# Optimization experiments

Measured on AMD Instinct MI355X. Metric: run time of the kernel, lower is better.

Reference implementation:

```python
import jax, jax.numpy as jnp
import numpy as np

B, T, LAGS, H, F = 4096, 256, 32, 128, 2


def setup_inputs() -> dict:
    key = jax.random.key(0)
    ks = jax.random.split(key, 6)
    s = lambda n: 1.0 / np.sqrt(n)
    return {
        "inputs": jax.random.normal(ks[0], (B, T, F), jnp.float32),
        "Wx": jax.random.normal(ks[1], (F, H), jnp.float32) * s(F),
        "Wh": jax.random.normal(ks[2], (H, H), jnp.float32) * s(H),
        "b": jnp.zeros((H,), jnp.float32),
        "Wd": jax.random.normal(ks[3], (H, 1), jnp.float32) * s(H),
        "bd": jnp.zeros((1,), jnp.float32),
        "alpha": jax.random.uniform(ks[4], (1, 1), jnp.float32),
        "lags": LAGS,
    }


def reference(inputs, Wx, Wh, b, Wd, bd, alpha, lags):
    # alpha constrained to [0, 1] (MinMax constraint / clamp in call)
    a = jnp.clip(alpha, 0.0, 1.0)  # [1,1]
    Bsz = inputs.shape[0]
    h0 = jnp.zeros((Bsz, Wh.shape[0]), inputs.dtype)

    def cell(h, x):
        # SimpleRNN cell: tanh(x Wx + h Wh + b)
        return jnp.tanh(x @ Wx + h @ Wh + b)

    # ---- warmup: run RNN over first `lags` steps of the full 2-feature input
    warm_xs = jnp.transpose(inputs[:, :lags], (1, 0, 2))  # [lags, B, F]

    def warm_step(h, x):
        return cell(h, x), None

    h, _ = jax.lax.scan(warm_step, h0, warm_xs)
    pred = h @ Wd + bd  # [B, 1] first prediction (appended un-smoothed)

    # step n consumes exogenous inputs[:, lags + n - 1, 0]
    exog = jnp.transpose(inputs[:, lags:-1, 0])  # [T-lags-1, B]

    def ar_step(carry, e):
        h, pred, es = carry
        x = jnp.concatenate([e[:, None], pred], axis=-1)  # [B, 2]
        h = cell(h, x)
        pred = h @ Wd + bd
        es = a * pred + (1.0 - a) * es  # exponential smoothing blend
        return (h, pred, es), es

    _, es_seq = jax.lax.scan(ar_step, (h, pred, pred), exog)  # [T-lags-1, B, 1]

    preds = jnp.concatenate([pred[None], es_seq], axis=0)  # [T-lags, B, 1]
    return jnp.transpose(preds, (1, 0, 2))  # [B, T-lags, 1]
```

## Files before the change

kernel.cpp:

```cpp
#include <hip/hip_runtime.h>

namespace {

constexpr int kB = 4096;
constexpr int kT = 256;
constexpr int kLags = 32;
constexpr int kH = 128;
constexpr int kSteps = 255;
constexpr int kOut = 224;
constexpr int kMT = 16;
constexpr int kThreads = 512;
constexpr int kHS = 136;
constexpr int kOS = 225;

constexpr float kZS = 2.8853900817779268f;

typedef __attribute__((ext_vector_type(8))) short short8;
typedef __attribute__((ext_vector_type(4))) float f32x4;

struct __align__(16) SMem {
    unsigned short hhi[2][kMT][kHS];
    unsigned short hlo[2][kMT][kHS];
    float x0T[kT][kMT];
    float x1wT[kLags][kMT];
    float obuf[kMT][kOS];
};

__device__ __forceinline__ unsigned short bf16_rne(float f) {
    unsigned u = __builtin_bit_cast(unsigned, f);
    u += 0x7FFFu + ((u >> 16) & 1u);
    return (unsigned short)(u >> 16);
}
__device__ __forceinline__ float bf16_f32(unsigned short h) {
    unsigned u = ((unsigned)h) << 16;
    return __builtin_bit_cast(float, u);
}
__device__ __forceinline__ float tanh_from_zs(float zs) {
    float e = __builtin_amdgcn_exp2f(zs);
    return fmaf(-2.0f, __builtin_amdgcn_rcpf(e + 1.0f), 1.0f);
}
__device__ __forceinline__ unsigned bf16_rne_hibits(float f) {
    unsigned u = __builtin_bit_cast(unsigned, f);
    return (u + (0x7FFFu + ((u >> 16) & 1u))) & 0xFFFF0000u;
}

__global__ __launch_bounds__(kThreads, 2)
void arx_rnn_es_kernel(const float* __restrict__ inputs,
                       const float* __restrict__ Wx,
                       const float* __restrict__ Wh,
                       const float* __restrict__ bias,
                       const float* __restrict__ Wd,
                       const float* __restrict__ bd,
                       const float* __restrict__ alpha,
                       float* __restrict__ out) {
    __shared__ SMem sm;
    const int tid  = threadIdx.x;
    const int b0   = blockIdx.x * kMT;
    const int lane = tid & 63;
    const int w    = tid >> 6;
    const int n    = lane & 15;
    const int q    = lane >> 4;

    for (int idx = tid; idx < kMT * kT; idx += kThreads) {
        const int mm = idx >> 8;
        const int t  = idx & 255;
        float2 v = ((const float2*)inputs)[(size_t)(b0 + mm) * kT + t];
        sm.x0T[t][mm] = v.x;
        if (t < kLags) sm.x1wT[t][mm] = v.y;
    }
    for (int idx = tid; idx < kMT * kHS; idx += kThreads) {
        ((unsigned short*)sm.hhi[0])[idx] = 0;
        ((unsigned short*)sm.hlo[0])[idx] = 0;
    }

    const float av  = fminf(fmaxf(alpha[0], 0.0f), 1.0f);
    const float bdv = bd[0];

    float sb2[4], swx0[4], swx1e[4], sbp[4];
#pragma unroll
    for (int r = 0; r < 4; ++r) {
        const int colE = w * 16 + q * 4 + r;
        const float bc = bias[colE];
        const float w0 = Wx[colE];
        const float w1 = Wx[kH + colE];
        sb2[r]   = kZS * bc;
        swx0[r]  = kZS * w0;
        swx1e[r] = kZS * w1;
        sbp[r]   = kZS * (bc + bdv * w1);
    }
    __syncthreads();

    int p = 0;

    {
        short8 whh[4], whl[4];
        {
            const int colw = w * 16 + n;
#pragma unroll
            for (int c = 0; c < 4; ++c) {
#pragma unroll
                for (int j = 0; j < 8; ++j) {
                    const int k = c * 32 + q * 8 + j;
                    float wv = kZS * Wh[(size_t)k * kH + colw];
                    unsigned short hi = bf16_rne(wv);
                    whh[c][j] = (short)hi;
                    whl[c][j] = (short)bf16_rne(wv - bf16_f32(hi));
                }
            }
        }

#pragma unroll 1
        for (int st = 0; st < kLags; ++st) {
            const float x0s = sm.x0T[st][n];
            const float x1s = sm.x1wT[st][n];

            short8 bh[4], bl[4];
#pragma unroll
            for (int c = 0; c < 4; ++c) {
                bh[c] = *(const short8*)&sm.hhi[p][n][c * 32 + 8 * q];
                bl[c] = *(const short8*)&sm.hlo[p][n][c * 32 + 8 * q];
            }

            f32x4 A = *(const f32x4*)&sb2[0];
#pragma unroll
            for (int c = 0; c < 4; ++c) {
                A = __builtin_amdgcn_mfma_f32_16x16x32_bf16(whh[c], bh[c], A, 0, 0, 0);
                A = __builtin_amdgcn_mfma_f32_16x16x32_bf16(whl[c], bh[c], A, 0, 0, 0);
                A = __builtin_amdgcn_mfma_f32_16x16x32_bf16(whh[c], bl[c], A, 0, 0, 0);
            }

            unsigned rb[4], db[4];
#pragma unroll
            for (int r = 0; r < 4; ++r) {
                float zs = A[r] + x0s * swx0[r] + x1s * swx1e[r];
                float hf = tanh_from_zs(zs);
                rb[r] = bf16_rne_hibits(hf);
                float d = hf - __builtin_bit_cast(float, rb[r]);
                db[r] = __builtin_bit_cast(unsigned, d);
            }
            uint2 uh, ul;
            uh.x = __builtin_amdgcn_perm(rb[1], rb[0], 0x07060302u);
            uh.y = __builtin_amdgcn_perm(rb[3], rb[2], 0x07060302u);
            ul.x = __builtin_amdgcn_perm(db[1], db[0], 0x07060302u);
            ul.y = __builtin_amdgcn_perm(db[3], db[2], 0x07060302u);
            const int wcol = w * 16 + q * 4;
            *(uint2*)&sm.hhi[1 - p][n][wcol] = uh;
            *(uint2*)&sm.hlo[1 - p][n][wcol] = ul;

            __syncthreads();
            p ^= 1;
        }
    }

    short8 fhh[4], fhl[4], dh[4];
    {
        const int colw = w * 16 + n;
        const float wx1w = Wx[kH + colw];
#pragma unroll
        for (int c = 0; c < 4; ++c) {
#pragma unroll
            for (int j = 0; j < 8; ++j) {
                const int k = c * 32 + q * 8 + j;
                float wv = kZS * fmaf(Wd[k], wx1w, Wh[(size_t)k * kH + colw]);
                unsigned short hi = bf16_rne(wv);
                fhh[c][j] = (short)hi;
                fhl[c][j] = (short)bf16_rne(wv - bf16_f32(hi));
                dh[c][j]  = (short)bf16_rne(Wd[k]);
            }
        }
    }

    float es = 0.0f;

#pragma unroll 1
    for (int st = kLags; st < kSteps; ++st) {
        const float x0s = sm.x0T[st][n];

        short8 bh[4], bl[4];
#pragma unroll
        for (int c = 0; c < 4; ++c) {
            bh[c] = *(const short8*)&sm.hhi[p][n][c * 32 + 8 * q];
            bl[c] = *(const short8*)&sm.hlo[p][n][c * 32 + 8 * q];
        }

        f32x4 A = *(const f32x4*)&sbp[0];
        f32x4 P = {0, 0, 0, 0};
#pragma unroll
        for (int c = 0; c < 4; ++c) {
            A = __builtin_amdgcn_mfma_f32_16x16x32_bf16(fhh[c], bh[c], A, 0, 0, 0);
            A = __builtin_amdgcn_mfma_f32_16x16x32_bf16(fhl[c], bh[c], A, 0, 0, 0);
            A = __builtin_amdgcn_mfma_f32_16x16x32_bf16(fhh[c], bl[c], A, 0, 0, 0);
            if (w == 0)
                P = __builtin_amdgcn_mfma_f32_16x16x32_bf16(dh[c], bh[c], P, 0, 0, 0);
        }

        if (w == 0 && q == 0) {
            float pv = P[0] + bdv;
            es = (st == kLags) ? pv : fmaf(av, pv - es, es);
            sm.obuf[n][st - kLags] = es;
        }

        unsigned rb[4], db[4];
#pragma unroll
        for (int r = 0; r < 4; ++r) {
            float zs = A[r] + x0s * swx0[r];
            float hf = tanh_from_zs(zs);
            rb[r] = bf16_rne_hibits(hf);
            float d = hf - __builtin_bit_cast(float, rb[r]);
            db[r] = __builtin_bit_cast(unsigned, d);
        }
        uint2 uh, ul;
        uh.x = __builtin_amdgcn_perm(rb[1], rb[0], 0x07060302u);
        uh.y = __builtin_amdgcn_perm(rb[3], rb[2], 0x07060302u);
        ul.x = __builtin_amdgcn_perm(db[1], db[0], 0x07060302u);
        ul.y = __builtin_amdgcn_perm(db[3], db[2], 0x07060302u);
        const int wcol = w * 16 + q * 4;
        *(uint2*)&sm.hhi[1 - p][n][wcol] = uh;
        *(uint2*)&sm.hlo[1 - p][n][wcol] = ul;

        __syncthreads();
        p ^= 1;
    }

    if (w == 0) {
        f32x4 P = {0, 0, 0, 0};
#pragma unroll
        for (int c = 0; c < 4; ++c) {
            short8 bh = *(const short8*)&sm.hhi[p][n][c * 32 + 8 * q];
            P = __builtin_amdgcn_mfma_f32_16x16x32_bf16(dh[c], bh, P, 0, 0, 0);
        }
        if (q == 0) {
            float pv = P[0] + bdv;
            es = fmaf(av, pv - es, es);
            sm.obuf[n][kOut - 1] = es;
        }
    }

    __syncthreads();
    for (int idx = tid; idx < kMT * kOut; idx += kThreads) {
        const int mm = idx / kOut;
        const int t  = idx - mm * kOut;
        out[(size_t)(b0 + mm) * kOut + t] = sm.obuf[mm][t];
    }
}

}

extern "C" void kernel_launch(void* const* d_in, const int* in_sizes, int n_in,
                              void* d_out, int out_size, void* d_ws, size_t ws_size,
                              hipStream_t stream) {
    const float* inputs = (const float*)d_in[0];
    const float* Wx     = (const float*)d_in[1];
    const float* Wh     = (const float*)d_in[2];
    const float* bias   = (const float*)d_in[3];
    const float* Wd     = (const float*)d_in[4];
    const float* bd     = (const float*)d_in[5];
    const float* alpha  = (const float*)d_in[6];

    arx_rnn_es_kernel<<<kB / kMT, kThreads, 0, stream>>>(
        inputs, Wx, Wh, bias, Wd, bd, alpha, (float*)d_out);
}
```

Before: 205.1 us.

## Halve block to four waves, split MFMA chains, distribute prediction dot across waves

The block shrinks from 8 to 4 waves, and each wave now computes 32 hidden columns as two 16-column tiles. Each step's MFMA work is split into three independent accumulator chains (hi*hi, lo*hi, hi*lo) with the input term folded into the initial accumulators, which shortens the dependent MFMA latency chain. The Wd output projection is spread across all four waves through a small shared partial-sum buffer, and the smoothing update lags one step behind. This cuts barrier participants and removes the wave-0-only serial prediction chain. In exchange each wave does more work per step, register pressure rises, and occupancy drops to one block of 4 waves per launch-bound hint.

```diff
diff --git a/kernel.cpp b/kernel.cpp
--- a/kernel.cpp
+++ b/kernel.cpp
@@ -9,9 +9,10 @@
 constexpr int kSteps = 255;
 constexpr int kOut = 224;
 constexpr int kMT = 16;
-constexpr int kThreads = 512;
+constexpr int kThreads = 256;
 constexpr int kHS = 136;
 constexpr int kOS = 225;
+constexpr int kHLO = 2 * kMT * kHS;
 
 constexpr float kZS = 2.8853900817779268f;
 
@@ -23,6 +24,7 @@
     unsigned short hlo[2][kMT][kHS];
     float x0T[kT][kMT];
     float x1wT[kLags][kMT];
+    float pbuf[2][4][kMT];
     float obuf[kMT][kOS];
 };
 
@@ -44,7 +46,7 @@
     return (u + (0x7FFFu + ((u >> 16) & 1u))) & 0xFFFF0000u;
 }
 
-__global__ __launch_bounds__(kThreads, 2)
+__global__ __launch_bounds__(kThreads, 1)
 void arx_rnn_es_kernel(const float* __restrict__ inputs,
                        const float* __restrict__ Wx,
                        const float* __restrict__ Wh,
@@ -76,26 +78,31 @@
     const float av  = fminf(fmaxf(alpha[0], 0.0f), 1.0f);
     const float bdv = bd[0];
 
-    float sb2[4], swx0[4], swx1e[4], sbp[4];
-#pragma unroll
-    for (int r = 0; r < 4; ++r) {
-        const int colE = w * 16 + q * 4 + r;
-        const float bc = bias[colE];
-        const float w0 = Wx[colE];
-        const float w1 = Wx[kH + colE];
-        sb2[r]   = kZS * bc;
-        swx0[r]  = kZS * w0;
-        swx1e[r] = kZS * w1;
-        sbp[r]   = kZS * (bc + bdv * w1);
+    f32x4 sb2v[2], swx0v[2], swx1ev[2], sbpv[2];
+#pragma unroll
+    for (int t = 0; t < 2; ++t) {
+#pragma unroll
+        for (int r = 0; r < 4; ++r) {
+            const int colE = w * 32 + t * 16 + q * 4 + r;
+            const float bc = bias[colE];
+            const float w0 = Wx[colE];
+            const float w1 = Wx[kH + colE];
+            sb2v[t][r]   = kZS * bc;
+            swx0v[t][r]  = kZS * w0;
+            swx1ev[t][r] = kZS * w1;
+            sbpv[t][r]   = kZS * (bc + bdv * w1);
+        }
     }
     __syncthreads();
 
+    const f32x4 zero4 = {0.0f, 0.0f, 0.0f, 0.0f};
     int p = 0;
 
     {
-        short8 whh[4], whl[4];
-        {
-            const int colw = w * 16 + n;
+        short8 whh[2][4], whl[2][4];
+#pragma unroll
+        for (int t = 0; t < 2; ++t) {
+            const int colw = w * 32 + t * 16 + n;
 #pragma unroll
             for (int c = 0; c < 4; ++c) {
 #pragma unroll
@@ -103,8 +110,8 @@
                     const int k = c * 32 + q * 8 + j;
                     float wv = kZS * Wh[(size_t)k * kH + colw];
                     unsigned short hi = bf16_rne(wv);
-                    whh[c][j] = (short)hi;
-                    whl[c][j] = (short)bf16_rne(wv - bf16_f32(hi));
+                    whh[t][c][j] = (short)hi;
+                    whl[t][c][j] = (short)bf16_rne(wv - bf16_f32(hi));
                 }
             }
         }
@@ -114,25 +121,133 @@
             const float x0s = sm.x0T[st][n];
             const float x1s = sm.x1wT[st][n];
 
+            const unsigned short* hb = (const unsigned short*)&sm.hhi[p][n][0];
+            unsigned short* hw = (unsigned short*)&sm.hhi[p ^ 1][n][0];
+
             short8 bh[4], bl[4];
 #pragma unroll
             for (int c = 0; c < 4; ++c) {
-                bh[c] = *(const short8*)&sm.hhi[p][n][c * 32 + 8 * q];
-                bl[c] = *(const short8*)&sm.hlo[p][n][c * 32 + 8 * q];
-            }
-
-            f32x4 A = *(const f32x4*)&sb2[0];
+                bh[c] = *(const short8*)(hb + c * 32 + 8 * q);
+                bl[c] = *(const short8*)(hb + kHLO + c * 32 + 8 * q);
+            }
+
+            f32x4 a1[2], a2[2], a3[2];
+#pragma unroll
+            for (int t = 0; t < 2; ++t) {
+                f32x4 xi;
+#pragma unroll
+                for (int r = 0; r < 4; ++r)
+                    xi[r] = fmaf(x0s, swx0v[t][r], x1s * swx1ev[t][r]);
+                a1[t] = __builtin_amdgcn_mfma_f32_16x16x32_bf16(whh[t][0], bh[0], sb2v[t], 0, 0, 0);
+                a2[t] = __builtin_amdgcn_mfma_f32_16x16x32_bf16(whl[t][0], bh[0], zero4,   0, 0, 0);
+                a3[t] = __builtin_amdgcn_mfma_f32_16x16x32_bf16(whh[t][0], bl[0], xi,      0, 0, 0);
+#pragma unroll
+                for (int c = 1; c < 4; ++c) {
+                    a1[t] = __builtin_amdgcn_mfma_f32_16x16x32_bf16(whh[t][c], bh[c], a1[t], 0, 0, 0);
+                    a2[t] = __builtin_amdgcn_mfma_f32_16x16x32_bf16(whl[t][c], bh[c], a2[t], 0, 0, 0);
+                    a3[t] = __builtin_amdgcn_mfma_f32_16x16x32_bf16(whh[t][c], bl[c], a3[t], 0, 0, 0);
+                }
+            }
+
+#pragma unroll
+            for (int t = 0; t < 2; ++t) {
+                unsigned rb[4], db[4];
+#pragma unroll
+                for (int r = 0; r < 4; ++r) {
+                    float zs = (a1[t][r] + a2[t][r]) + a3[t][r];
+                    float hf = tanh_from_zs(zs);
+                    rb[r] = bf16_rne_hibits(hf);
+                    float d = hf - __builtin_bit_cast(float, rb[r]);
+                    db[r] = __builtin_bit_cast(unsigned, d);
+                }
+                uint2 uh, ul;
+                uh.x = __builtin_amdgcn_perm(rb[1], rb[0], 0x07060302u);
+                uh.y = __builtin_amdgcn_perm(rb[3], rb[2], 0x07060302u);
+                ul.x = __builtin_amdgcn_perm(db[1], db[0], 0x07060302u);
+                ul.y = __builtin_amdgcn_perm(db[3], db[2], 0x07060302u);
+                *(uint2*)(hw + w * 32 + t * 16 + q * 4) = uh;
+                *(uint2*)(hw + kHLO + w * 32 + t * 16 + q * 4) = ul;
+            }
+
+            __syncthreads();
+            p ^= 1;
+        }
+    }
+
+    short8 fhh[2][4], fhl[2][4], dhw;
+    {
+#pragma unroll
+        for (int t = 0; t < 2; ++t) {
+            const int colw = w * 32 + t * 16 + n;
+            const float wx1w = Wx[kH + colw];
 #pragma unroll
             for (int c = 0; c < 4; ++c) {
-                A = __builtin_amdgcn_mfma_f32_16x16x32_bf16(whh[c], bh[c], A, 0, 0, 0);
-                A = __builtin_amdgcn_mfma_f32_16x16x32_bf16(whl[c], bh[c], A, 0, 0, 0);
-                A = __builtin_amdgcn_mfma_f32_16x16x32_bf16(whh[c], bl[c], A, 0, 0, 0);
-            }
-
+#pragma unroll
+                for (int j = 0; j < 8; ++j) {
+                    const int k = c * 32 + q * 8 + j;
+                    float wv = kZS * fmaf(Wd[k], wx1w, Wh[(size_t)k * kH + colw]);
+                    unsigned short hi = bf16_rne(wv);
+                    fhh[t][c][j] = (short)hi;
+                    fhl[t][c][j] = (short)bf16_rne(wv - bf16_f32(hi));
+                }
+            }
+        }
+#pragma unroll
+        for (int j = 0; j < 8; ++j)
+            dhw[j] = (short)bf16_rne(Wd[w * 32 + q * 8 + j]);
+    }
+
+    float es = 0.0f;
+
+#pragma unroll 1
+    for (int st = kLags; st < kSteps; ++st) {
+        const float x0s = sm.x0T[st][n];
+
+        const unsigned short* hb = (const unsigned short*)&sm.hhi[p][n][0];
+        unsigned short* hw = (unsigned short*)&sm.hhi[p ^ 1][n][0];
+
+        short8 bh[4], bl[4];
+#pragma unroll
+        for (int c = 0; c < 4; ++c) {
+            bh[c] = *(const short8*)(hb + c * 32 + 8 * q);
+            bl[c] = *(const short8*)(hb + kHLO + c * 32 + 8 * q);
+        }
+        short8 bhP = *(const short8*)(hb + w * 32 + 8 * q);
+
+        f32x4 a1[2], a2[2], a3[2];
+#pragma unroll
+        for (int t = 0; t < 2; ++t) {
+            f32x4 xi;
+#pragma unroll
+            for (int r = 0; r < 4; ++r) xi[r] = x0s * swx0v[t][r];
+            a1[t] = __builtin_amdgcn_mfma_f32_16x16x32_bf16(fhh[t][0], bh[0], sbpv[t], 0, 0, 0);
+            a2[t] = __builtin_amdgcn_mfma_f32_16x16x32_bf16(fhl[t][0], bh[0], zero4,   0, 0, 0);
+            a3[t] = __builtin_amdgcn_mfma_f32_16x16x32_bf16(fhh[t][0], bl[0], xi,      0, 0, 0);
+#pragma unroll
+            for (int c = 1; c < 4; ++c) {
+                a1[t] = __builtin_amdgcn_mfma_f32_16x16x32_bf16(fhh[t][c], bh[c], a1[t], 0, 0, 0);
+                a2[t] = __builtin_amdgcn_mfma_f32_16x16x32_bf16(fhl[t][c], bh[c], a2[t], 0, 0, 0);
+                a3[t] = __builtin_amdgcn_mfma_f32_16x16x32_bf16(fhh[t][c], bl[c], a3[t], 0, 0, 0);
+            }
+        }
+
+        f32x4 P = __builtin_amdgcn_mfma_f32_16x16x32_bf16(dhw, bhP, zero4, 0, 0, 0);
+        if (q == 0) sm.pbuf[p][w][n] = P[0];
+
+        if (w == 0 && q == 0 && st > kLags) {
+            float pv = ((sm.pbuf[p ^ 1][0][n] + sm.pbuf[p ^ 1][1][n]) +
+                        (sm.pbuf[p ^ 1][2][n] + sm.pbuf[p ^ 1][3][n])) + bdv;
+            const int m = st - kLags - 1;
+            es = (m == 0) ? pv : fmaf(av, pv - es, es);
+            sm.obuf[n][m] = es;
+        }
+
+#pragma unroll
+        for (int t = 0; t < 2; ++t) {
             unsigned rb[4], db[4];
 #pragma unroll
             for (int r = 0; r < 4; ++r) {
-                float zs = A[r] + x0s * swx0[r] + x1s * swx1e[r];
+                float zs = (a1[t][r] + a2[t][r]) + a3[t][r];
                 float hf = tanh_from_zs(zs);
                 rb[r] = bf16_rne_hibits(hf);
                 float d = hf - __builtin_bit_cast(float, rb[r]);
@@ -143,97 +258,32 @@
             uh.y = __builtin_amdgcn_perm(rb[3], rb[2], 0x07060302u);
             ul.x = __builtin_amdgcn_perm(db[1], db[0], 0x07060302u);
             ul.y = __builtin_amdgcn_perm(db[3], db[2], 0x07060302u);
-            const int wcol = w * 16 + q * 4;
-            *(uint2*)&sm.hhi[1 - p][n][wcol] = uh;
-            *(uint2*)&sm.hlo[1 - p][n][wcol] = ul;
-
-            __syncthreads();
-            p ^= 1;
-        }
-    }
-
-    short8 fhh[4], fhl[4], dh[4];
-    {
-        const int colw = w * 16 + n;
-        const float wx1w = Wx[kH + colw];
-#pragma unroll
-        for (int c = 0; c < 4; ++c) {
-#pragma unroll
-            for (int j = 0; j < 8; ++j) {
-                const int k = c * 32 + q * 8 + j;
-                float wv = kZS * fmaf(Wd[k], wx1w, Wh[(size_t)k * kH + colw]);
-                unsigned short hi = bf16_rne(wv);
-                fhh[c][j] = (short)hi;
-                fhl[c][j] = (short)bf16_rne(wv - bf16_f32(hi));
-                dh[c][j]  = (short)bf16_rne(Wd[k]);
-            }
-        }
-    }
-
-    float es = 0.0f;
-
-#pragma unroll 1
-    for (int st = kLags; st < kSteps; ++st) {
-        const float x0s = sm.x0T[st][n];
-
-        short8 bh[4], bl[4];
-#pragma unroll
-        for (int c = 0; c < 4; ++c) {
-            bh[c] = *(const short8*)&sm.hhi[p][n][c * 32 + 8 * q];
-            bl[c] = *(const short8*)&sm.hlo[p][n][c * 32 + 8 * q];
-        }
-
-        f32x4 A = *(const f32x4*)&sbp[0];
-        f32x4 P = {0, 0, 0, 0};
-#pragma unroll
-        for (int c = 0; c < 4; ++c) {
-            A = __builtin_amdgcn_mfma_f32_16x16x32_bf16(fhh[c], bh[c], A, 0, 0, 0);
-            A = __builtin_amdgcn_mfma_f32_16x16x32_bf16(fhl[c], bh[c], A, 0, 0, 0);
-            A = __builtin_amdgcn_mfma_f32_16x16x32_bf16(fhh[c], bl[c], A, 0, 0, 0);
-            if (w == 0)
-                P = __builtin_amdgcn_mfma_f32_16x16x32_bf16(dh[c], bh[c], P, 0, 0, 0);
-        }
-
-        if (w == 0 && q == 0) {
-            float pv = P[0] + bdv;
-            es = (st == kLags) ? pv : fmaf(av, pv - es, es);
-            sm.obuf[n][st - kLags] = es;
-        }
-
-        unsigned rb[4], db[4];
-#pragma unroll
-        for (int r = 0; r < 4; ++r) {
-            float zs = A[r] + x0s * swx0[r];
-            float hf = tanh_from_zs(zs);
-            rb[r] = bf16_rne_hibits(hf);
-            float d = hf - __builtin_bit_cast(float, rb[r]);
-            db[r] = __builtin_bit_cast(unsigned, d);
-        }
-        uint2 uh, ul;
-        uh.x = __builtin_amdgcn_perm(rb[1], rb[0], 0x07060302u);
-        uh.y = __builtin_amdgcn_perm(rb[3], rb[2], 0x07060302u);
-        ul.x = __builtin_amdgcn_perm(db[1], db[0], 0x07060302u);
-        ul.y = __builtin_amdgcn_perm(db[3], db[2], 0x07060302u);
-        const int wcol = w * 16 + q * 4;
-        *(uint2*)&sm.hhi[1 - p][n][wcol] = uh;
-        *(uint2*)&sm.hlo[1 - p][n][wcol] = ul;
+            *(uint2*)(hw + w * 32 + t * 16 + q * 4) = uh;
+            *(uint2*)(hw + kHLO + w * 32 + t * 16 + q * 4) = ul;
+        }
 
         __syncthreads();
         p ^= 1;
     }
 
-    if (w == 0) {
-        f32x4 P = {0, 0, 0, 0};
-#pragma unroll
-        for (int c = 0; c < 4; ++c) {
-            short8 bh = *(const short8*)&sm.hhi[p][n][c * 32 + 8 * q];
-            P = __builtin_amdgcn_mfma_f32_16x16x32_bf16(dh[c], bh, P, 0, 0, 0);
-        }
-        if (q == 0) {
-            float pv = P[0] + bdv;
-            es = fmaf(av, pv - es, es);
-            sm.obuf[n][kOut - 1] = es;
-        }
+    if (w == 0 && q == 0) {
+        float pv = ((sm.pbuf[p ^ 1][0][n] + sm.pbuf[p ^ 1][1][n]) +
+                    (sm.pbuf[p ^ 1][2][n] + sm.pbuf[p ^ 1][3][n])) + bdv;
+        es = fmaf(av, pv - es, es);
+        sm.obuf[n][kOut - 2] = es;
+    }
+    {
+        const unsigned short* hb = (const unsigned short*)&sm.hhi[p][n][0];
+        short8 bhP = *(const short8*)(hb + w * 32 + 8 * q);
+        f32x4 P = __builtin_amdgcn_mfma_f32_16x16x32_bf16(dhw, bhP, zero4, 0, 0, 0);
+        if (q == 0) sm.pbuf[p][w][n] = P[0];
+    }
+    __syncthreads();
+    if (w == 0 && q == 0) {
+        float pv = ((sm.pbuf[p][0][n] + sm.pbuf[p][1][n]) +
+                    (sm.pbuf[p][2][n] + sm.pbuf[p][3][n])) + bdv;
+        es = fmaf(av, pv - es, es);
+        sm.obuf[n][kOut - 1] = es;
     }
 
     __syncthreads();
```

After: 252.4 us. +23.1%, slower.
